# Kernel optimization log

Hardware: AMD Instinct MI355X
Metric: run time of the kernel (lower is better)

## Reference

```python
import jax, jax.numpy as jnp
import numpy as np

B, LQ, LK = 128, 512, 512
QS, KS, AS = 256, 256, 64


def setup_inputs() -> dict:
    key = jax.random.key(0)
    ks = jax.random.split(key, 7)
    s = 0.05
    return {
        "queries": jax.random.normal(ks[0], (B, LQ, QS), dtype=jnp.float32),
        "keys": jax.random.normal(ks[1], (B, LK, KS), dtype=jnp.float32),
        "w_relation": jax.random.normal(ks[2], (QS, KS), dtype=jnp.float32) * s,
        "W_q": jax.random.normal(ks[3], (QS, AS), dtype=jnp.float32) * s,
        "W_k": jax.random.normal(ks[4], (KS, AS), dtype=jnp.float32) * s,
        "W_q_att": jax.random.normal(ks[5], (AS, 1), dtype=jnp.float32) * s,
        "W_k_att": jax.random.normal(ks[6], (AS, 1), dtype=jnp.float32) * s,
    }


def reference(queries, keys, w_relation, W_q, W_k, W_q_att, W_k_att):
    # relation_scores: [B, Lq, Lk]
    rel = jnp.tanh(jnp.einsum("bqd,de,bke->bqk", queries, w_relation, keys))
    q_proj = jnp.einsum("bqd,da->bqa", queries, W_q)   # [B, Lq, A]
    k_proj = jnp.einsum("bkd,da->bka", keys, W_k)      # [B, Lk, A]
    q_att_score = jnp.tanh(q_proj + jnp.einsum("bqk,bka->bqa", rel, k_proj))
    k_att_score = jnp.tanh(k_proj + jnp.einsum("bqk,bqa->bka", rel, q_proj))
    # softmax over the sequence dim (dim=1)
    q_att_w = jax.nn.softmax(q_att_score @ W_q_att, axis=1)  # [B, Lq, 1]
    k_att_w = jax.nn.softmax(k_att_score @ W_k_att, axis=1)  # [B, Lk, 1]
    weighted_queries = q_att_w * queries
    weighted_keys = k_att_w * keys
    return (weighted_queries, weighted_keys, q_att_w, k_att_w)
```

## Files before the change

### kernel.cpp

```cpp
#include <hip/hip_runtime.h>
#include <math.h>


#define SEQ 512
#define DIM 256
#define ADIM 64
#define OUT_QATT ((size_t)33554432)

using hfrag = __attribute__((ext_vector_type(8))) _Float16;
using s4 = __attribute__((ext_vector_type(4))) short;
using f4 = __attribute__((ext_vector_type(4))) float;
typedef unsigned int u32;

__device__ __forceinline__ void gl_lds16(const short* g, short* l) {
  __builtin_amdgcn_global_load_lds((const __attribute__((address_space(1))) u32*)g,
                                   (__attribute__((address_space(3))) u32*)l, 16, 0, 0);
}

__device__ __forceinline__ short f2h(float x) {
  _Float16 h = (_Float16)x;
  return __builtin_bit_cast(short, h);
}
__device__ __forceinline__ float h2f(short s) {
  return (float)__builtin_bit_cast(_Float16, s);
}
__device__ __forceinline__ float tanhf_fast(float x) {
  float e = __expf(2.0f * x);
  return 1.0f - 2.0f / (e + 1.0f);
}


template <int KTOT>
__device__ __forceinline__ void core128(const short* __restrict__ A,
                                        const short* __restrict__ Bt,
                                        short* sA, short* sB, f4 acc[4][4]) {
  const int t = threadIdx.x;
  const int lane = t & 63, wave = t >> 6;
  const int wm = (wave & 1) << 6, wn = (wave >> 1) << 6;
  const int l15 = lane & 15, qd = lane >> 4;
  const int srow = t >> 3, scol = (t & 7) << 3;
  for (int k0 = 0; k0 < KTOT; k0 += 64) {
#pragma unroll
    for (int i = 0; i < 4; i++) {
      const int row = srow + (i << 5);
      const int gcol = k0 + (scol ^ ((row & 7) << 3));
      gl_lds16(&A[(size_t)row * KTOT + gcol], &sA[t * 8 + i * 2048]);
      gl_lds16(&Bt[(size_t)row * KTOT + gcol], &sB[t * 8 + i * 2048]);
    }
    __syncthreads();
#pragma unroll
    for (int ks = 0; ks < 2; ks++) {
      hfrag af[4], bg[4];
      const int kk = (ks << 5) + (qd << 3);
#pragma unroll
      for (int i = 0; i < 4; i++) {
        const int ar = wm + (i << 4) + l15;
        const int br = wn + (i << 4) + l15;
        af[i] = *(const hfrag*)&sA[(ar << 6) + (kk ^ ((ar & 7) << 3))];
        bg[i] = *(const hfrag*)&sB[(br << 6) + (kk ^ ((br & 7) << 3))];
      }
#pragma unroll
      for (int i = 0; i < 4; i++)
#pragma unroll
        for (int j = 0; j < 4; j++)
          acc[i][j] = __builtin_amdgcn_mfma_f32_16x16x32_f16(af[i], bg[j], acc[i][j], 0, 0, 0);
    }
    __syncthreads();
  }
}

template <int KTOT>
__device__ __forceinline__ void core64(const short* __restrict__ A,
                                       const short* __restrict__ Bt,
                                       short* sA, short* sB, f4 acc[4][2]) {
  const int t = threadIdx.x;
  const int lane = t & 63, wave = t >> 6;
  const int wm = (wave & 1) << 6, wn = (wave >> 1) << 5;
  const int l15 = lane & 15, qd = lane >> 4;
  const int srow = t >> 3, scol = (t & 7) << 3;
  for (int k0 = 0; k0 < KTOT; k0 += 64) {
#pragma unroll
    for (int i = 0; i < 4; i++) {
      const int row = srow + (i << 5);
      const int gcol = k0 + (scol ^ ((row & 7) << 3));
      gl_lds16(&A[(size_t)row * KTOT + gcol], &sA[t * 8 + i * 2048]);
      if (i < 2) gl_lds16(&Bt[(size_t)row * KTOT + gcol], &sB[t * 8 + i * 2048]);
    }
    __syncthreads();
#pragma unroll
    for (int ks = 0; ks < 2; ks++) {
      hfrag af[4], bg[2];
      const int kk = (ks << 5) + (qd << 3);
#pragma unroll
      for (int i = 0; i < 4; i++) {
        const int ar = wm + (i << 4) + l15;
        af[i] = *(const hfrag*)&sA[(ar << 6) + (kk ^ ((ar & 7) << 3))];
      }
#pragma unroll
      for (int j = 0; j < 2; j++) {
        const int br = wn + (j << 4) + l15;
        bg[j] = *(const hfrag*)&sB[(br << 6) + (kk ^ ((br & 7) << 3))];
      }
#pragma unroll
      for (int i = 0; i < 4; i++)
#pragma unroll
        for (int j = 0; j < 2; j++)
          acc[i][j] = __builtin_amdgcn_mfma_f32_16x16x32_f16(af[i], bg[j], acc[i][j], 0, 0, 0);
    }
    __syncthreads();
  }
}


__global__ __launch_bounds__(256) void cvt_kernel(const float* __restrict__ Q,
                                                  const float* __restrict__ K,
                                                  const float* __restrict__ wrel,
                                                  const float* __restrict__ Wq,
                                                  const float* __restrict__ Wk,
                                                  short* __restrict__ Qh, short* __restrict__ Kh,
                                                  short* __restrict__ wrelT,
                                                  short* __restrict__ WqT,
                                                  short* __restrict__ WkT) {
  const int bid = blockIdx.x;
  if (bid < 32768) {
    const size_t g = ((size_t)bid << 8) + threadIdx.x;
    const int side = (int)(g >> 22);
    const size_t loc = g & 4194303;
    const float4 v = ((const float4*)(side ? K : Q))[loc];
    s4 o;
    o[0] = f2h(v.x); o[1] = f2h(v.y); o[2] = f2h(v.z); o[3] = f2h(v.w);
    *(s4*)&(side ? Kh : Qh)[loc << 2] = o;
  } else {
    const int b2 = bid - 32768;
    if (b2 < 64) {
      const int i = (b2 << 8) + threadIdx.x;
#pragma unroll
      for (int u = 0; u < 4; u++) {
        const int idx = (i << 2) + u;
        const int e = idx >> 8, d = idx & 255;
        wrelT[idx] = f2h(wrel[(d << 8) + e]);
      }
    } else if (b2 < 72) {
      const int i = ((b2 - 64) << 8) + threadIdx.x;
#pragma unroll
      for (int u = 0; u < 8; u++) {
        const int idx = (i << 3) + u;
        const int a = idx >> 8, d = idx & 255;
        WqT[idx] = f2h(Wq[(d << 6) + a]);
      }
    } else if (b2 < 80) {
      const int i = ((b2 - 72) << 8) + threadIdx.x;
#pragma unroll
      for (int u = 0; u < 8; u++) {
        const int idx = (i << 3) + u;
        const int a = idx >> 8, d = idx & 255;
        WkT[idx] = f2h(Wk[(d << 6) + a]);
      }
    }
  }
}

__global__ __launch_bounds__(256) void proj_kernel(const short* __restrict__ Qh,
                                                   const short* __restrict__ Kh,
                                                   const short* __restrict__ WqT,
                                                   const short* __restrict__ WkT,
                                                   short* __restrict__ qp, short* __restrict__ kp,
                                                   short* __restrict__ qpT, short* __restrict__ kpT) {
  __shared__ short sA[8192];
  __shared__ short sB[4096];
  const int which = blockIdx.y;
  const short* A = which ? Kh : Qh;
  const short* Bt = which ? WkT : WqT;
  short* P = which ? kp : qp;
  short* PT = which ? kpT : qpT;
  const int m0 = blockIdx.x << 7;
  f4 acc[4][2];
  const f4 fz = {0.f, 0.f, 0.f, 0.f};
#pragma unroll
  for (int i = 0; i < 4; i++)
#pragma unroll
    for (int j = 0; j < 2; j++) acc[i][j] = fz;
  core64<256>(A + (size_t)m0 * 256, Bt, sA, sB, acc);
  const int lane = threadIdx.x & 63, wave = threadIdx.x >> 6;
  const int wm = (wave & 1) << 6, wn = (wave >> 1) << 5;
  const int l15 = lane & 15, qd = lane >> 4;
#pragma unroll
  for (int i = 0; i < 4; i++)
#pragma unroll
    for (int j = 0; j < 2; j++) {
      s4 pack;
      const int gm0 = m0 + wm + (i << 4) + (qd << 2);
      const int a = wn + (j << 4) + l15;
#pragma unroll
      for (int r = 0; r < 4; r++) {
        pack[r] = f2h(acc[i][j][r]);
        P[(size_t)(gm0 + r) * ADIM + a] = pack[r];
      }
      const int bb = gm0 >> 9, ql = gm0 & 511;
      *(s4*)&PT[((size_t)bb * ADIM + a) * SEQ + ql] = pack;
    }
}

__global__ __launch_bounds__(256) void qw_kernel(const short* __restrict__ Qh,
                                                 const short* __restrict__ WrT,
                                                 short* __restrict__ qw) {
  __shared__ short sA[8192];
  __shared__ short sB[8192];
  const int m0 = blockIdx.x << 7, n0 = blockIdx.y << 7;
  f4 acc[4][4];
  const f4 fz = {0.f, 0.f, 0.f, 0.f};
#pragma unroll
  for (int i = 0; i < 4; i++)
#pragma unroll
    for (int j = 0; j < 4; j++) acc[i][j] = fz;
  core128<256>(Qh + (size_t)m0 * 256, WrT + (size_t)n0 * 256, sA, sB, acc);
  const int lane = threadIdx.x & 63, wave = threadIdx.x >> 6;
  const int wm = (wave & 1) << 6, wn = (wave >> 1) << 6;
  const int l15 = lane & 15, qd = lane >> 4;
#pragma unroll
  for (int i = 0; i < 4; i++)
#pragma unroll
    for (int j = 0; j < 4; j++)
#pragma unroll
      for (int r = 0; r < 4; r++) {
        const int row = m0 + wm + (i << 4) + (qd << 2) + r;
        const int col = n0 + wn + (j << 4) + l15;
        qw[(size_t)row * 256 + col] = f2h(acc[i][j][r]);
      }
}

__global__ __launch_bounds__(256) void rel_mfma(const short* __restrict__ qw,
                                                const short* __restrict__ Kh,
                                                short* __restrict__ rel,
                                                short* __restrict__ relT) {
  __shared__ short sA[8192];
  __shared__ short sB[8192];
  const int b = blockIdx.z;
  const int m0 = blockIdx.x << 7, n0 = blockIdx.y << 7;
  f4 acc[4][4];
  const f4 fz = {0.f, 0.f, 0.f, 0.f};
#pragma unroll
  for (int i = 0; i < 4; i++)
#pragma unroll
    for (int j = 0; j < 4; j++) acc[i][j] = fz;
  core128<256>(qw + ((size_t)b * SEQ + m0) * 256, Kh + ((size_t)b * SEQ + n0) * 256, sA, sB, acc);
  short* R = rel + (size_t)b * SEQ * SEQ;
  short* RT = relT + (size_t)b * SEQ * SEQ;
  const int lane = threadIdx.x & 63, wave = threadIdx.x >> 6;
  const int wm = (wave & 1) << 6, wn = (wave >> 1) << 6;
  const int l15 = lane & 15, qd = lane >> 4;
#pragma unroll
  for (int i = 0; i < 4; i++)
#pragma unroll
    for (int j = 0; j < 4; j++) {
      s4 pack;
      const int row0 = m0 + wm + (i << 4) + (qd << 2);
      const int col = n0 + wn + (j << 4) + l15;
#pragma unroll
      for (int r = 0; r < 4; r++) {
        pack[r] = f2h(tanhf_fast(acc[i][j][r]));
        R[(size_t)(row0 + r) * SEQ + col] = pack[r];
      }
      *(s4*)&RT[(size_t)col * SEQ + row0] = pack;
    }
}

__global__ __launch_bounds__(256) void acc_kernel(const short* __restrict__ Rel,
                                                  const short* __restrict__ Pt,
                                                  const short* __restrict__ Prm,
                                                  const float* __restrict__ Watt,
                                                  float* __restrict__ logit, int gb0) {
  __shared__ short sA[8192];
  __shared__ short sB[4096];
  __shared__ float lbuf[128][2];
  const int b = blockIdx.y, gb = gb0 + b;
  const int m0 = blockIdx.x << 7;
  f4 acc[4][2];
  const f4 fz = {0.f, 0.f, 0.f, 0.f};
#pragma unroll
  for (int i = 0; i < 4; i++)
#pragma unroll
    for (int j = 0; j < 2; j++) acc[i][j] = fz;
  core64<512>(Rel + (size_t)b * SEQ * SEQ + (size_t)m0 * SEQ, Pt + (size_t)gb * ADIM * SEQ,
              sA, sB, acc);
  const int lane = threadIdx.x & 63, wave = threadIdx.x >> 6;
  const int wm = (wave & 1) << 6, wn = (wave >> 1) << 5;
  const int l15 = lane & 15, qd = lane >> 4;
  float p[4][4];
#pragma unroll
  for (int i = 0; i < 4; i++)
#pragma unroll
    for (int r = 0; r < 4; r++) p[i][r] = 0.f;
#pragma unroll
  for (int i = 0; i < 4; i++)
#pragma unroll
    for (int r = 0; r < 4; r++) {
      const int gm = gb * SEQ + m0 + wm + (i << 4) + (qd << 2) + r;
#pragma unroll
      for (int j = 0; j < 2; j++) {
        const int a = wn + (j << 4) + l15;
        const float s = tanhf_fast(h2f(Prm[(size_t)gm * ADIM + a]) + acc[i][j][r]);
        p[i][r] += s * Watt[a];
      }
    }
#pragma unroll
  for (int off = 8; off; off >>= 1)
#pragma unroll
    for (int i = 0; i < 4; i++)
#pragma unroll
      for (int r = 0; r < 4; r++) p[i][r] += __shfl_down(p[i][r], off, 16);
  if (l15 == 0) {
#pragma unroll
    for (int i = 0; i < 4; i++)
#pragma unroll
      for (int r = 0; r < 4; r++) lbuf[wm + (i << 4) + (qd << 2) + r][wave >> 1] = p[i][r];
  }
  __syncthreads();
  const int t = threadIdx.x;
  if (t < 128) logit[(size_t)gb * SEQ + m0 + t] = lbuf[t][0] + lbuf[t][1];
}

__global__ __launch_bounds__(256) void softmax_kernel(const float* __restrict__ qlog,
                                                      const float* __restrict__ klog,
                                                      float* __restrict__ out) {
  const int bx = blockIdx.x;
  const int side = bx >> 7;
  const int b = bx & 127;
  const float* lg = (side ? klog : qlog) + (size_t)b * SEQ;
  float* o = out + OUT_QATT + (size_t)side * (128 * SEQ) + (size_t)b * SEQ;
  const int t = threadIdx.x;
  float v0 = lg[t];
  float v1 = lg[t + 256];
  float m = fmaxf(v0, v1);
#pragma unroll
  for (int off = 32; off; off >>= 1) m = fmaxf(m, __shfl_xor(m, off));
  __shared__ float sm[4], ss[4];
  const int w = t >> 6, l = t & 63;
  if (l == 0) sm[w] = m;
  __syncthreads();
  m = fmaxf(fmaxf(sm[0], sm[1]), fmaxf(sm[2], sm[3]));
  float e0 = expf(v0 - m), e1 = expf(v1 - m);
  float s = e0 + e1;
#pragma unroll
  for (int off = 32; off; off >>= 1) s += __shfl_xor(s, off);
  if (l == 0) ss[w] = s;
  __syncthreads();
  s = ss[0] + ss[1] + ss[2] + ss[3];
  float inv = 1.0f / s;
  o[t] = e0 * inv;
  o[t + 256] = e1 * inv;
}

__global__ __launch_bounds__(256) void weight_kernel(const float* __restrict__ queries,
                                                     const float* __restrict__ keys,
                                                     float* __restrict__ out) {
  const size_t g = (size_t)blockIdx.x * 256 + threadIdx.x;
  const int side = (int)(g >> 22);
  const size_t loc = g & 4194303;
  const size_t row = loc >> 6;
  const float* aw = out + OUT_QATT + (size_t)side * (128 * SEQ);
  const float4* src = (const float4*)(side ? keys : queries);
  const float w = aw[row];
  float4 v = src[loc];
  float4 r = {v.x * w, v.y * w, v.z * w, v.w * w};
  ((float4*)out)[g] = r;
}

extern "C" void kernel_launch(void* const* d_in, const int* in_sizes, int n_in,
                              void* d_out, int out_size, void* d_ws, size_t ws_size,
                              hipStream_t stream) {
  const float* queries = (const float*)d_in[0];
  const float* keys = (const float*)d_in[1];
  const float* w_rel = (const float*)d_in[2];
  const float* W_q = (const float*)d_in[3];
  const float* W_k = (const float*)d_in[4];
  const float* W_qa = (const float*)d_in[5];
  const float* W_ka = (const float*)d_in[6];
  float* out = (float*)d_out;

  short* Qh = (short*)d_ws;
  short* Kh = Qh + 16777216;
  short* qp = Kh + 16777216;
  short* kp = qp + 4194304;
  float* qlog = (float*)(kp + 4194304);
  float* klog = qlog + 65536;

  char* ob = (char*)d_out;
  short* rel_s = (short*)ob;
  short* relT_s = (short*)(ob + 33554432);
  short* qw_s = (short*)(ob + 67108864);
  short* qpT = (short*)(ob + 83886080);
  short* kpT = (short*)(ob + 92274688);
  short* wrelT = (short*)(ob + 100663296);
  short* WqT = (short*)(ob + 100794368);
  short* WkT = (short*)(ob + 100827136);

  cvt_kernel<<<32848, 256, 0, stream>>>(queries, keys, w_rel, W_q, W_k, Qh, Kh, wrelT, WqT, WkT);
  proj_kernel<<<dim3(512, 2), 256, 0, stream>>>(Qh, Kh, WqT, WkT, qp, kp, qpT, kpT);

  for (int s = 0; s < 2; s++) {
    const int gb0 = s * 64;
    qw_kernel<<<dim3(256, 2), 256, 0, stream>>>(Qh + (size_t)gb0 * SEQ * DIM, wrelT, qw_s);
    rel_mfma<<<dim3(4, 4, 64), 256, 0, stream>>>(qw_s, Kh + (size_t)gb0 * SEQ * DIM, rel_s, relT_s);
    acc_kernel<<<dim3(4, 64), 256, 0, stream>>>(rel_s, kpT, qp, W_qa, qlog, gb0);
    acc_kernel<<<dim3(4, 64), 256, 0, stream>>>(relT_s, qpT, kp, W_ka, klog, gb0);
  }

  softmax_kernel<<<256, 256, 0, stream>>>(qlog, klog, out);
  weight_kernel<<<32768, 256, 0, stream>>>(queries, keys, out);
}
```

Measured before the change: 423.3 us.

## Fuse relation tanh tile with both attention accumulations, avoiding global rel matrices

Replaces the rel_mfma and two acc_kernel launches with one fused kernel. Each block computes a 128x128 tanh relation tile, stages it and its transpose in swizzled LDS, and immediately multiplies it by the k and q projections. The q-side logit is finished in-block, while per-tile k-side partials go to a global buffer that a new klog_kernel reduces. This removes the round trip of the two 32 MB fp16 relation matrices and the two-pass batch split, at the cost of a larger kpart scratch buffer, 64 KB of LDS per block and a grid of only 512 blocks.

New measurement: 450.8 us. +6.5%, slower.

```diff
diff --git a/kernel.cpp b/kernel.cpp
--- a/kernel.cpp
+++ b/kernel.cpp
@@ -229,95 +229,155 @@
       }
 }
 
-__global__ __launch_bounds__(256) void rel_mfma(const short* __restrict__ qw,
-                                                const short* __restrict__ Kh,
-                                                short* __restrict__ rel,
-                                                short* __restrict__ relT) {
-  __shared__ short sA[8192];
-  __shared__ short sB[8192];
-  const int b = blockIdx.z;
-  const int m0 = blockIdx.x << 7, n0 = blockIdx.y << 7;
-  f4 acc[4][4];
+__global__ __launch_bounds__(256) void fused_kernel(const short* __restrict__ qw,
+                                                    const short* __restrict__ Kh,
+                                                    const short* __restrict__ qpT,
+                                                    const short* __restrict__ kpT,
+                                                    const short* __restrict__ qp,
+                                                    const float* __restrict__ Wqa,
+                                                    float* __restrict__ kpart,
+                                                    float* __restrict__ qlog) {
+  __shared__ short smem[32768];
+  short* sA = smem;
+  short* sB = smem + 8192;
+  short* tile = smem;
+  short* tileT = smem + 16384;
+  const int mt = blockIdx.x, b = blockIdx.y;
+  const int t = threadIdx.x;
+  const int lane = t & 63, wave = t >> 6;
+  const int l15 = lane & 15, qd = lane >> 4;
+  const int wm = (wave & 1) << 6, wn = (wave >> 1) << 6;
+  const int rbase = wave << 5;
   const f4 fz = {0.f, 0.f, 0.f, 0.f};
-#pragma unroll
-  for (int i = 0; i < 4; i++)
-#pragma unroll
-    for (int j = 0; j < 4; j++) acc[i][j] = fz;
-  core128<256>(qw + ((size_t)b * SEQ + m0) * 256, Kh + ((size_t)b * SEQ + n0) * 256, sA, sB, acc);
-  short* R = rel + (size_t)b * SEQ * SEQ;
-  short* RT = relT + (size_t)b * SEQ * SEQ;
-  const int lane = threadIdx.x & 63, wave = threadIdx.x >> 6;
-  const int wm = (wave & 1) << 6, wn = (wave >> 1) << 6;
-  const int l15 = lane & 15, qd = lane >> 4;
-#pragma unroll
-  for (int i = 0; i < 4; i++)
-#pragma unroll
-    for (int j = 0; j < 4; j++) {
-      s4 pack;
-      const int row0 = m0 + wm + (i << 4) + (qd << 2);
-      const int col = n0 + wn + (j << 4) + l15;
+
+  f4 qacc[2][4];
+#pragma unroll
+  for (int i2 = 0; i2 < 2; i2++)
+#pragma unroll
+    for (int j2 = 0; j2 < 4; j2++) qacc[i2][j2] = fz;
+
+  const short* kpT_b = kpT + ((size_t)b * ADIM) * SEQ;
+  const short* qpT_b = qpT + ((size_t)b * ADIM) * SEQ;
+
+  for (int n0 = 0; n0 < 4; n0++) {
+    f4 acc[4][4];
+#pragma unroll
+    for (int i = 0; i < 4; i++)
+#pragma unroll
+      for (int j = 0; j < 4; j++) acc[i][j] = fz;
+    core128<256>(qw + ((size_t)b * SEQ + mt * 128) * 256,
+                 Kh + ((size_t)b * SEQ + n0 * 128) * 256, sA, sB, acc);
+#pragma unroll
+    for (int i = 0; i < 4; i++)
+#pragma unroll
+      for (int j = 0; j < 4; j++) {
+        const int row0 = wm + (i << 4) + (qd << 2);
+        const int col = wn + (j << 4) + l15;
+        s4 pack;
+#pragma unroll
+        for (int r = 0; r < 4; r++) {
+          const short h = f2h(tanhf_fast(acc[i][j][r]));
+          pack[r] = h;
+          const int row = row0 + r;
+          tile[(row << 7) + (col ^ ((row & 7) << 3))] = h;
+        }
+        *(s4*)&tileT[(col << 7) + (row0 ^ ((col & 7) << 3))] = pack;
+      }
+    __syncthreads();
+    f4 kacc[2][4];
+#pragma unroll
+    for (int i2 = 0; i2 < 2; i2++)
+#pragma unroll
+      for (int j2 = 0; j2 < 4; j2++) kacc[i2][j2] = fz;
+#pragma unroll
+    for (int ks = 0; ks < 4; ks++) {
+      const int kkk = (ks << 5) + (qd << 3);
+      hfrag aq[2], ak[2], bq[4], bk[4];
+#pragma unroll
+      for (int i2 = 0; i2 < 2; i2++) {
+        const int ar = rbase + (i2 << 4) + l15;
+        aq[i2] = *(const hfrag*)&tile[(ar << 7) + (kkk ^ ((ar & 7) << 3))];
+        ak[i2] = *(const hfrag*)&tileT[(ar << 7) + (kkk ^ ((ar & 7) << 3))];
+      }
+#pragma unroll
+      for (int j2 = 0; j2 < 4; j2++) {
+        const int a = (j2 << 4) + l15;
+        bq[j2] = *(const hfrag*)&kpT_b[(size_t)a * SEQ + (n0 << 7) + kkk];
+        bk[j2] = *(const hfrag*)&qpT_b[(size_t)a * SEQ + (mt << 7) + kkk];
+      }
+#pragma unroll
+      for (int i2 = 0; i2 < 2; i2++)
+#pragma unroll
+        for (int j2 = 0; j2 < 4; j2++) {
+          qacc[i2][j2] = __builtin_amdgcn_mfma_f32_16x16x32_f16(aq[i2], bq[j2], qacc[i2][j2], 0, 0, 0);
+          kacc[i2][j2] = __builtin_amdgcn_mfma_f32_16x16x32_f16(ak[i2], bk[j2], kacc[i2][j2], 0, 0, 0);
+        }
+    }
+#pragma unroll
+    for (int i2 = 0; i2 < 2; i2++)
+#pragma unroll
+      for (int j2 = 0; j2 < 4; j2++) {
+        const int krow = (n0 << 7) + rbase + (i2 << 4) + (qd << 2);
+        const int a = (j2 << 4) + l15;
+#pragma unroll
+        for (int r = 0; r < 4; r++)
+          kpart[((((size_t)b << 2) + mt) * SEQ + krow + r) * ADIM + a] = kacc[i2][j2][r];
+      }
+    __syncthreads();
+  }
+  float p[2][4];
+#pragma unroll
+  for (int i2 = 0; i2 < 2; i2++)
+#pragma unroll
+    for (int r = 0; r < 4; r++) p[i2][r] = 0.f;
+#pragma unroll
+  for (int i2 = 0; i2 < 2; i2++)
+#pragma unroll
+    for (int r = 0; r < 4; r++) {
+      const int q = (mt << 7) + rbase + (i2 << 4) + (qd << 2) + r;
+      const size_t gq = (size_t)b * SEQ + q;
+#pragma unroll
+      for (int j2 = 0; j2 < 4; j2++) {
+        const int a = (j2 << 4) + l15;
+        p[i2][r] += tanhf_fast(h2f(qp[gq * ADIM + a]) + qacc[i2][j2][r]) * Wqa[a];
+      }
+    }
+#pragma unroll
+  for (int off = 8; off; off >>= 1)
+#pragma unroll
+    for (int i2 = 0; i2 < 2; i2++)
+#pragma unroll
+      for (int r = 0; r < 4; r++) p[i2][r] += __shfl_down(p[i2][r], off, 16);
+  if (l15 == 0) {
+#pragma unroll
+    for (int i2 = 0; i2 < 2; i2++)
 #pragma unroll
       for (int r = 0; r < 4; r++) {
-        pack[r] = f2h(tanhf_fast(acc[i][j][r]));
-        R[(size_t)(row0 + r) * SEQ + col] = pack[r];
-      }
-      *(s4*)&RT[(size_t)col * SEQ + row0] = pack;
-    }
-}
-
-__global__ __launch_bounds__(256) void acc_kernel(const short* __restrict__ Rel,
-                                                  const short* __restrict__ Pt,
-                                                  const short* __restrict__ Prm,
-                                                  const float* __restrict__ Watt,
-                                                  float* __restrict__ logit, int gb0) {
-  __shared__ short sA[8192];
-  __shared__ short sB[4096];
-  __shared__ float lbuf[128][2];
-  const int b = blockIdx.y, gb = gb0 + b;
-  const int m0 = blockIdx.x << 7;
-  f4 acc[4][2];
-  const f4 fz = {0.f, 0.f, 0.f, 0.f};
-#pragma unroll
-  for (int i = 0; i < 4; i++)
-#pragma unroll
-    for (int j = 0; j < 2; j++) acc[i][j] = fz;
-  core64<512>(Rel + (size_t)b * SEQ * SEQ + (size_t)m0 * SEQ, Pt + (size_t)gb * ADIM * SEQ,
-              sA, sB, acc);
-  const int lane = threadIdx.x & 63, wave = threadIdx.x >> 6;
-  const int wm = (wave & 1) << 6, wn = (wave >> 1) << 5;
-  const int l15 = lane & 15, qd = lane >> 4;
-  float p[4][4];
-#pragma unroll
-  for (int i = 0; i < 4; i++)
-#pragma unroll
-    for (int r = 0; r < 4; r++) p[i][r] = 0.f;
-#pragma unroll
-  for (int i = 0; i < 4; i++)
-#pragma unroll
-    for (int r = 0; r < 4; r++) {
-      const int gm = gb * SEQ + m0 + wm + (i << 4) + (qd << 2) + r;
-#pragma unroll
-      for (int j = 0; j < 2; j++) {
-        const int a = wn + (j << 4) + l15;
-        const float s = tanhf_fast(h2f(Prm[(size_t)gm * ADIM + a]) + acc[i][j][r]);
-        p[i][r] += s * Watt[a];
-      }
-    }
-#pragma unroll
-  for (int off = 8; off; off >>= 1)
-#pragma unroll
-    for (int i = 0; i < 4; i++)
-#pragma unroll
-      for (int r = 0; r < 4; r++) p[i][r] += __shfl_down(p[i][r], off, 16);
-  if (l15 == 0) {
-#pragma unroll
-    for (int i = 0; i < 4; i++)
-#pragma unroll
-      for (int r = 0; r < 4; r++) lbuf[wm + (i << 4) + (qd << 2) + r][wave >> 1] = p[i][r];
-  }
-  __syncthreads();
-  const int t = threadIdx.x;
-  if (t < 128) logit[(size_t)gb * SEQ + m0 + t] = lbuf[t][0] + lbuf[t][1];
+        const int q = (mt << 7) + rbase + (i2 << 4) + (qd << 2) + r;
+        qlog[(size_t)b * SEQ + q] = p[i2][r];
+      }
+  }
+}
+
+__global__ __launch_bounds__(256) void klog_kernel(const float* __restrict__ kpart,
+                                                   const short* __restrict__ kp,
+                                                   const float* __restrict__ Wka,
+                                                   float* __restrict__ klog) {
+  const int half = blockIdx.x, b = blockIdx.y;
+  const int t = threadIdx.x, a = t & 63, wave = t >> 6;
+  const float w = Wka[a];
+  const int kbase = (half << 8) + (wave << 6);
+  const size_t pb = ((size_t)b << 2) * SEQ * ADIM;
+  for (int it = 0; it < 64; it++) {
+    const int k = kbase + it;
+    const size_t base = pb + (size_t)k * ADIM + a;
+    float s = kpart[base] + kpart[base + (size_t)SEQ * ADIM] +
+              kpart[base + (size_t)2 * SEQ * ADIM] + kpart[base + (size_t)3 * SEQ * ADIM];
+    s = tanhf_fast(s + h2f(kp[((size_t)b * SEQ + k) * ADIM + a])) * w;
+#pragma unroll
+    for (int off = 32; off; off >>= 1) s += __shfl_xor(s, off);
+    if (a == 0) klog[(size_t)b * SEQ + k] = s;
+  }
 }
 
 __global__ __launch_bounds__(256) void softmax_kernel(const float* __restrict__ qlog,
@@ -386,26 +446,19 @@
   float* klog = qlog + 65536;
 
   char* ob = (char*)d_out;
-  short* rel_s = (short*)ob;
-  short* relT_s = (short*)(ob + 33554432);
-  short* qw_s = (short*)(ob + 67108864);
-  short* qpT = (short*)(ob + 83886080);
-  short* kpT = (short*)(ob + 92274688);
-  short* wrelT = (short*)(ob + 100663296);
-  short* WqT = (short*)(ob + 100794368);
-  short* WkT = (short*)(ob + 100827136);
+  short* qw_s = (short*)ob;
+  float* kpart = (float*)(ob + 33554432);
+  short* qpT = (short*)(ob + 100663296);
+  short* kpT = (short*)(ob + 109051904);
+  short* wrelT = (short*)(ob + 117440512);
+  short* WqT = (short*)(ob + 117571584);
+  short* WkT = (short*)(ob + 117604352);
 
   cvt_kernel<<<32848, 256, 0, stream>>>(queries, keys, w_rel, W_q, W_k, Qh, Kh, wrelT, WqT, WkT);
   proj_kernel<<<dim3(512, 2), 256, 0, stream>>>(Qh, Kh, WqT, WkT, qp, kp, qpT, kpT);
-
-  for (int s = 0; s < 2; s++) {
-    const int gb0 = s * 64;
-    qw_kernel<<<dim3(256, 2), 256, 0, stream>>>(Qh + (size_t)gb0 * SEQ * DIM, wrelT, qw_s);
-    rel_mfma<<<dim3(4, 4, 64), 256, 0, stream>>>(qw_s, Kh + (size_t)gb0 * SEQ * DIM, rel_s, relT_s);
-    acc_kernel<<<dim3(4, 64), 256, 0, stream>>>(rel_s, kpT, qp, W_qa, qlog, gb0);
-    acc_kernel<<<dim3(4, 64), 256, 0, stream>>>(relT_s, qpT, kp, W_ka, klog, gb0);
-  }
-
+  qw_kernel<<<dim3(512, 2), 256, 0, stream>>>(Qh, wrelT, qw_s);
+  fused_kernel<<<dim3(4, 128), 256, 0, stream>>>(qw_s, Kh, qpT, kpT, qp, W_qa, kpart, qlog);
+  klog_kernel<<<dim3(2, 128), 256, 0, stream>>>(kpart, kp, W_ka, klog);
   softmax_kernel<<<256, 256, 0, stream>>>(qlog, klog, out);
   weight_kernel<<<32768, 256, 0, stream>>>(queries, keys, out);
 }
```
